# Kernel tuning notes

Hardware: AMD Instinct MI355X
Metric: run time of the kernel (lower is better)

## Reference

```python
import jax, jax.numpy as jnp
import numpy as np

N_QUBITS = 12
N_LAYERS = 6
BATCH = 2048
N_OUTPUTS = 2
C64 = jnp.complex64


def setup_inputs() -> dict:
    key = jax.random.key(0)
    k1, k2 = jax.random.split(key)
    x = jax.random.normal(k1, (BATCH, N_QUBITS), dtype=jnp.float32)
    # nn.Parameter: torch.randn(n_layers, n_qubits, 3) * 0.1
    weights = jax.random.normal(k2, (N_LAYERS, N_QUBITS, 3), dtype=jnp.float32) * 0.1
    return {"x": x, "weights": weights}


def _rx(t):
    # t: (...,) angles -> (..., 2, 2) RX matrices
    c = jnp.cos(t * 0.5).astype(C64)
    s = (-1j * jnp.sin(t * 0.5)).astype(C64)
    return jnp.stack([jnp.stack([c, s], -1), jnp.stack([s, c], -1)], -2)


def _ry(t):
    c = jnp.cos(t * 0.5).astype(C64)
    s = jnp.sin(t * 0.5).astype(C64)
    return jnp.stack([jnp.stack([c, -s], -1), jnp.stack([s, c], -1)], -2)


def _rz(t):
    e = jnp.exp(-0.5j * t).astype(C64)
    z = jnp.zeros_like(e)
    return jnp.stack([jnp.stack([e, z], -1), jnp.stack([z, jnp.conj(e)], -1)], -2)


def _rot(w):
    # PennyLane Rot(phi, theta, omega) = RZ(omega) @ RY(theta) @ RZ(phi); w: (n_qubits, 3)
    return _rz(w[:, 2]) @ _ry(w[:, 1]) @ _rz(w[:, 0])


def _apply_1q(state, gate, q):
    # state: (B, 2**n) complex; gate: (2,2) or (B,2,2); qubit q (wire 0 = MSB)
    B = state.shape[0]
    s = state.reshape(B, 2 ** q, 2, -1)
    if gate.ndim == 3:
        s = jnp.einsum('bij,bljr->blir', gate, s)
    else:
        s = jnp.einsum('ij,bljr->blir', gate, s)
    return s.reshape(B, -1)


def _apply_cnot(state, c, t, n):
    # control c, target t; flip target axis where control bit == 1
    B = state.shape[0]
    s = state.reshape((B,) + (2,) * n)
    ac, at = 1 + c, 1 + t
    s0 = jnp.take(s, 0, axis=ac)
    s1 = jnp.take(s, 1, axis=ac)
    at2 = at - 1 if at > ac else at
    s1 = jnp.flip(s1, axis=at2)
    s = jnp.stack([s0, s1], axis=ac)
    return s.reshape(B, -1)


def _layer(state, w, n):
    # strongly-entangling layer: Rot on every wire, then full CNOT entanglement
    rot = _rot(w)  # (n, 2, 2)
    for q in range(n):
        state = _apply_1q(state, rot[q], q)
    for i in range(n):
        for j in range(i + 1, n):
            state = _apply_cnot(state, i, j, n)
    return state


def _forward(x, weights):
    n = N_QUBITS
    B = x.shape[0]
    state = jnp.zeros((B, 2 ** n), C64).at[:, 0].set(1.0)
    # angle encoding: RX(x_q) on wire q (PennyLane AngleEmbedding default axis X)
    for q in range(n):
        state = _apply_1q(state, _rx(x[:, q]), q)
    layer_ckpt = jax.checkpoint(lambda s, w: _layer(s, w, n))
    for l in range(N_LAYERS):
        state = layer_ckpt(state, weights[l])
    # expval(PauliZ) on wires 0..n_outputs-1
    probs = state.real ** 2 + state.imag ** 2  # (B, 2**n)
    outs = []
    for k in range(N_OUTPUTS):
        p = probs.reshape(B, 2 ** k, 2, -1)
        outs.append(p[:, :, 0, :].sum((1, 2)) - p[:, :, 1, :].sum((1, 2)))
    return jnp.stack(outs, -1)  # (B, n_outputs)


def reference(x, weights):
    return _forward(x, weights)
```

## Files before the change

### kernel.cpp

```cpp
#include <hip/hip_runtime.h>
#include <math.h>

#define NQ 12
#define DIM 4096
#define NL 6
#define TPB 64


#define WS_WA0 0
#define WS_Z0  128
#define WS_W   256
#define WS_Z   896
#define WS_RYT 2176

typedef float f2 __attribute__((ext_vector_type(2)));

__device__ __forceinline__ f2 pk_mul(f2 a, f2 b) {
  f2 d; asm("v_pk_mul_f32 %0, %1, %2" : "=v"(d) : "v"(a), "v"(b)); return d;
}
__device__ __forceinline__ f2 pk_fma(f2 a, f2 b, f2 c) {
  f2 d; asm("v_pk_fma_f32 %0, %1, %2, %3" : "=v"(d) : "v"(a), "v"(b), "v"(c)); return d;
}
__device__ __forceinline__ f2 cmulp(f2 a, f2 c) {
  f2 r1, d;
  asm("v_pk_mul_f32 %0, %1, %2 op_sel:[0,0] op_sel_hi:[0,1]"
      : "=v"(r1) : "v"(a), "v"(c));
  asm("v_pk_fma_f32 %0, %1, %2, %3 op_sel:[1,1,0] op_sel_hi:[1,0,1] neg_lo:[1,0,0]"
      : "=v"(d) : "v"(a), "v"(c), "v"(r1));
  return d;
}

template<int BIT>
__device__ __forceinline__ void apply_ry64(f2 v[64], f2 cc, f2 ss) {
  #pragma unroll
  for (int j = 0; j < 64; ++j) {
    if (j & (1 << BIT)) continue;
    const int k = j | (1 << BIT);
    f2 a = v[j], b = v[k];
    f2 t1 = pk_mul(a, cc);
    f2 t2 = pk_mul(a, ss);
    f2 na; asm("v_pk_fma_f32 %0, %1, %2, %3 neg_lo:[1,0,0] neg_hi:[1,0,0]"
               : "=v"(na) : "v"(b), "v"(ss), "v"(t1));
    f2 nb = pk_fma(b, cc, t2);
    v[j] = na; v[k] = nb;
  }
}

__global__ __launch_bounds__(256)
void qprep_kernel(const float* __restrict__ w, float* __restrict__ ws) {
  const int t = threadIdx.x;
  const float HPI = 1.57079632679489662f;

  if (t < 64) {
    const int u = t;
    float f = 0.f;
    #pragma unroll
    for (int k = 0; k < 6; ++k) {
      float p = w[(0*NQ + (11-k))*3 + 0];
      f += ((u >> k) & 1) ? 0.5f*p : -0.5f*p;
    }
    f -= HPI * (float)__popc(u);
    float sv, cv; sincosf(f, &sv, &cv);
    ws[WS_WA0 + 2*u] = cv; ws[WS_WA0 + 2*u + 1] = sv;
  } else if (t < 128) {
    const int p_ = t - 64;
    float f = 0.f;
    #pragma unroll
    for (int k = 0; k < 6; ++k) {
      float p = w[(0*NQ + (5-k))*3 + 0];
      f += ((p_ >> k) & 1) ? 0.5f*p : -0.5f*p;
    }
    f -= HPI * (float)__popc(p_);
    float sv, cv; sincosf(f, &sv, &cv);
    ws[WS_Z0 + 2*p_] = cv; ws[WS_Z0 + 2*p_ + 1] = sv;
  }

  for (int idx = t; idx < 5*64; idx += 256) {
    const int l = idx >> 6, u = idx & 63;
    float f = 0.f;
    #pragma unroll
    for (int k = 0; k < 6; ++k) {
      float om = w[(l*NQ + (5-k))*3 + 2];
      f += ((u >> k) & 1) ? 0.5f*om : -0.5f*om;
    }
    const int gu = u ^ (u >> 1);
    #pragma unroll
    for (int k = 0; k < 6; ++k) {
      float ph = w[((l+1)*NQ + (5-k))*3 + 0];
      f += ((gu >> k) & 1) ? 0.5f*ph : -0.5f*ph;
    }
    float sv, cv; sincosf(f, &sv, &cv);
    ws[WS_W + 2*idx] = cv; ws[WS_W + 2*idx + 1] = sv;
  }

  for (int idx = t; idx < 5*2*64; idx += 256) {
    const int l = idx >> 7, h = (idx >> 6) & 1, p_ = idx & 63;
    float f = 0.f;
    #pragma unroll
    for (int k = 0; k < 6; ++k) {
      float om = w[(l*NQ + (11-k))*3 + 2];
      f += ((p_ >> k) & 1) ? 0.5f*om : -0.5f*om;
    }
    const int gp = (p_ ^ (p_ >> 1)) ^ (h << 5);
    #pragma unroll
    for (int k = 0; k < 6; ++k) {
      float ph = w[((l+1)*NQ + (11-k))*3 + 0];
      f += ((gp >> k) & 1) ? 0.5f*ph : -0.5f*ph;
    }
    float sv, cv; sincosf(f, &sv, &cv);
    ws[WS_Z + 2*idx] = cv; ws[WS_Z + 2*idx + 1] = sv;
  }

  if (t < NL*NQ) {
    float sv, cv; sincosf(0.5f*w[t*3 + 1], &sv, &cv);
    ((float4*)(ws + WS_RYT))[t] = make_float4(cv, cv, sv, sv);
  }
}

__global__ __launch_bounds__(TPB, 1)
void qsim12_kernel(const float* __restrict__ x, const float* __restrict__ ws,
                   float* __restrict__ out) {
  __shared__ __align__(16) float st[2*DIM];
  const int L = threadIdx.x;
  const int b = blockIdx.x;
  char* stb = (char*)st;

  float csx[NQ], csy[NQ];
  {
    float xv = (L < NQ) ? x[b*NQ + L] : 0.f;
    float sv, cv; sincosf(0.5f*xv, &sv, &cv);
    #pragma unroll
    for (int q = 0; q < NQ; ++q) {
      csx[q] = __int_as_float(__builtin_amdgcn_readlane(__float_as_int(cv), q));
      csy[q] = __int_as_float(__builtin_amdgcn_readlane(__float_as_int(sv), q));
    }
  }

  f2 v[64];

  {
    float rl = 1.f;
    #pragma unroll
    for (int k = 0; k < 6; ++k)
      rl *= ((L >> k) & 1) ? csy[11-k] : csx[11-k];
    float mlo[8], mhi[8];
    #pragma unroll
    for (int pm = 0; pm < 8; ++pm) {
      float a = ((pm >> 0) & 1) ? csy[5] : csx[5];
      a *= ((pm >> 1) & 1) ? csy[4] : csx[4];
      a *= ((pm >> 2) & 1) ? csy[3] : csx[3];
      mlo[pm] = a;
      float bb = ((pm >> 0) & 1) ? csy[2] : csx[2];
      bb *= ((pm >> 1) & 1) ? csy[1] : csx[1];
      bb *= ((pm >> 2) & 1) ? csy[0] : csx[0];
      mhi[pm] = bb;
    }
    const float2 wv = *(const float2*)(ws + WS_WA0 + 2*L);
    const f2 a0 = (f2){wv.x*rl, wv.y*rl};
    #pragma unroll
    for (int p = 0; p < 64; ++p) {
      const float2 zv = *(const float2*)(ws + WS_Z0 + 2*p);
      f2 ph = cmulp(a0, (f2){zv.x, zv.y});
      const float m = mlo[p & 7] * mhi[p >> 3];
      v[p] = pk_mul(ph, (f2){m, m});
    }
  }

  #define RY6(BIT, WQ) { const float4 r = *(const float4*)(ws + WS_RYT + 4*(l*NQ + (WQ))); \
      apply_ry64<BIT>(v, (f2){r.x, r.y}, (f2){r.z, r.w}); }

  #pragma unroll 1
  for (int l = 0; l < NL; ++l) {
    if (l > 0) {
      #pragma unroll
      for (int r = 0; r < 64; ++r)
        v[r] = *(const f2*)(stb + r*512 + ((L ^ (r & 62)) << 3));
    }
    RY6(0,5) RY6(1,4) RY6(2,3) RY6(3,2) RY6(4,1) RY6(5,0)

    #pragma unroll
    for (int m = 0; m < 32; ++m) {
      const int idx = (2*m) ^ (L & 62);
      *(float4*)(stb + L*512 + (idx << 3)) =
          make_float4(v[2*m].x, v[2*m].y, v[2*m+1].x, v[2*m+1].y);
    }
    __syncthreads();
    #pragma unroll
    for (int p = 0; p < 64; ++p)
      v[p] = *(const f2*)(stb + p*512 + ((L ^ (p & 62)) << 3));

    RY6(0,11) RY6(1,10) RY6(2,9) RY6(3,8) RY6(4,7) RY6(5,6)

    if (l < NL-1) {
      const float2 wv = *(const float2*)(ws + WS_W + (l*64 + L)*2);
      const f2 W = (f2){wv.x, wv.y};
      const float* zb = ws + WS_Z + ((l*2 + (L & 1))*64)*2;
      #pragma unroll
      for (int p0 = 0; p0 < 64; p0 += 8) {
        f2 z[8];
        #pragma unroll
        for (int q = 0; q < 8; ++q) {
          const float2 zv = *(const float2*)(zb + 2*(p0+q));
          z[q] = (f2){zv.x, zv.y};
        }
        #pragma unroll
        for (int q = 0; q < 8; ++q)
          v[p0+q] = cmulp(cmulp(v[p0+q], z[q]), W);
      }
      __syncthreads();

      const int Gh  = (L ^ (L >> 1)) & 63;
      const int hb5 = (L & 1) << 5;
      const int gsw = Gh & 62;
      #pragma unroll
      for (int m = 0; m < 32; ++m) {
        const int glo0 = ((2*m) ^ m) ^ hb5;
        const int e = glo0 & ~1;
        float4 q4;
        if (m & 1) q4 = make_float4(v[2*m+1].x, v[2*m+1].y, v[2*m].x, v[2*m].y);
        else       q4 = make_float4(v[2*m].x, v[2*m].y, v[2*m+1].x, v[2*m+1].y);
        *(float4*)(stb + Gh*512 + ((e ^ gsw) << 3)) = q4;
      }
      __syncthreads();
    }
  }

  float ssum = 0.f;
  #pragma unroll
  for (int p = 0; p < 64; ++p)
    ssum += v[p].x*v[p].x + v[p].y*v[p].y;
  float s0 = ((L >> 5) & 1) ? -ssum : ssum;
  float s1 = (((L >> 4) ^ (L >> 5)) & 1) ? -ssum : ssum;
  #pragma unroll
  for (int off = 32; off >= 1; off >>= 1) {
    s0 += __shfl_down(s0, off);
    s1 += __shfl_down(s1, off);
  }
  if (L == 0) { out[b*2 + 0] = s0; out[b*2 + 1] = s1; }
}

extern "C" void kernel_launch(void* const* d_in, const int* in_sizes, int n_in,
                              void* d_out, int out_size, void* d_ws, size_t ws_size,
                              hipStream_t stream) {
  const float* x = (const float*)d_in[0];
  const float* w = (const float*)d_in[1];
  float* out = (float*)d_out;
  float* ws = (float*)d_ws;
  int B = in_sizes[0] / NQ;
  qprep_kernel<<<1, 256, 0, stream>>>(w, ws);
  qsim12_kernel<<<B, TPB, 0, stream>>>(x, ws, out);
}
```

Baseline: 155.3 us.

## Replace shared-memory transposes with ds_bpermute cross-lane permutations

Both transposes between the low and high qubit halves now use per-register ds_bpermute lane shuffles, and so does the Gray-code CNOT permutation. That removes the shared-memory state buffer and the __syncthreads barriers. The Z phase table is copied into a small LDS array, and launch bounds are raised to 2 blocks per CU to improve occupancy. The RY update is reformulated with a lane-dependent sign so that each step maps onto the bpermute layout. Each bpermute of a complex value costs two LDS-path instructions, so there are many more of them per layer, and register pressure at the higher occupancy may cause spills.

Result: slower. 207.2 us (+33.4%).

```diff
diff --git a/kernel.cpp b/kernel.cpp
--- a/kernel.cpp
+++ b/kernel.cpp
@@ -2,7 +2,6 @@
 #include <math.h>
 
 #define NQ 12
-#define DIM 4096
 #define NL 6
 #define TPB 64
 
@@ -15,13 +14,13 @@
 
 typedef float f2 __attribute__((ext_vector_type(2)));
 
-__device__ __forceinline__ f2 pk_mul(f2 a, f2 b) {
+static __device__ __forceinline__ f2 pk_mul(f2 a, f2 b) {
   f2 d; asm("v_pk_mul_f32 %0, %1, %2" : "=v"(d) : "v"(a), "v"(b)); return d;
 }
-__device__ __forceinline__ f2 pk_fma(f2 a, f2 b, f2 c) {
+static __device__ __forceinline__ f2 pk_fma(f2 a, f2 b, f2 c) {
   f2 d; asm("v_pk_fma_f32 %0, %1, %2, %3" : "=v"(d) : "v"(a), "v"(b), "v"(c)); return d;
 }
-__device__ __forceinline__ f2 cmulp(f2 a, f2 c) {
+static __device__ __forceinline__ f2 cmulp(f2 a, f2 c) {
   f2 r1, d;
   asm("v_pk_mul_f32 %0, %1, %2 op_sel:[0,0] op_sel_hi:[0,1]"
       : "=v"(r1) : "v"(a), "v"(c));
@@ -29,20 +28,27 @@
       : "=v"(d) : "v"(a), "v"(c), "v"(r1));
   return d;
 }
+static __device__ __forceinline__ f2 bp2(int addr, f2 s) {
+  f2 d;
+  d.x = __int_as_float(__builtin_amdgcn_ds_bpermute(addr, __float_as_int(s.x)));
+  d.y = __int_as_float(__builtin_amdgcn_ds_bpermute(addr, __float_as_int(s.y)));
+  return d;
+}
 
 template<int BIT>
-__device__ __forceinline__ void apply_ry64(f2 v[64], f2 cc, f2 ss) {
+static __device__ __forceinline__ void apply_ry64(f2 v[64], f2 cc, f2 SS) {
   #pragma unroll
   for (int j = 0; j < 64; ++j) {
     if (j & (1 << BIT)) continue;
     const int k = j | (1 << BIT);
     f2 a = v[j], b = v[k];
     f2 t1 = pk_mul(a, cc);
-    f2 t2 = pk_mul(a, ss);
-    f2 na; asm("v_pk_fma_f32 %0, %1, %2, %3 neg_lo:[1,0,0] neg_hi:[1,0,0]"
-               : "=v"(na) : "v"(b), "v"(ss), "v"(t1));
-    f2 nb = pk_fma(b, cc, t2);
-    v[j] = na; v[k] = nb;
+    f2 t2 = pk_mul(b, cc);
+    v[j] = pk_fma(b, SS, t1);
+    f2 nb;
+    asm("v_pk_fma_f32 %0, %1, %2, %3 neg_lo:[1,0,0] neg_hi:[1,0,0]"
+        : "=v"(nb) : "v"(a), "v"(SS), "v"(t2));
+    v[k] = nb;
   }
 }
 
@@ -117,13 +123,24 @@
   }
 }
 
-__global__ __launch_bounds__(TPB, 1)
+#define STEP(DST, SRC) v[DST] = bp2(vgi ^ ((SRC) << 2), v[SRC]);
+#define CYC2(A,B) { f2 t_ = v[A]; STEP(A,B); v[B] = bp2(vgi ^ ((A) << 2), t_); }
+#define CYC4(A,B,C,D) { f2 t_ = v[A]; STEP(A,B); STEP(B,C); STEP(C,D); \
+                        v[D] = bp2(vgi ^ ((A) << 2), t_); }
+#define CYC8(A,B,C,D,E,F,G,H) { f2 t_ = v[A]; STEP(A,B); STEP(B,C); STEP(C,D); \
+                        STEP(D,E); STEP(E,F); STEP(F,G); STEP(G,H); \
+                        v[H] = bp2(vgi ^ ((A) << 2), t_); }
+
+__global__ __launch_bounds__(TPB, 2)
 void qsim12_kernel(const float* __restrict__ x, const float* __restrict__ ws,
                    float* __restrict__ out) {
-  __shared__ __align__(16) float st[2*DIM];
+  __shared__ __align__(16) float zt[5*2*64*2];
   const int L = threadIdx.x;
   const int b = blockIdx.x;
-  char* stb = (char*)st;
+
+  #pragma unroll
+  for (int i = 0; i < 10; ++i)
+    ((f2*)zt)[i*64 + L] = *(const f2*)(ws + WS_Z + 2*(i*64 + L));
 
   float csx[NQ], csy[NQ];
   {
@@ -137,91 +154,72 @@
   }
 
   f2 v[64];
+  const int lb = L << 2;
 
   {
     float rl = 1.f;
     #pragma unroll
     for (int k = 0; k < 6; ++k)
       rl *= ((L >> k) & 1) ? csy[11-k] : csx[11-k];
-    float mlo[8], mhi[8];
-    #pragma unroll
-    for (int pm = 0; pm < 8; ++pm) {
-      float a = ((pm >> 0) & 1) ? csy[5] : csx[5];
-      a *= ((pm >> 1) & 1) ? csy[4] : csx[4];
-      a *= ((pm >> 2) & 1) ? csy[3] : csx[3];
-      mlo[pm] = a;
-      float bb = ((pm >> 0) & 1) ? csy[2] : csx[2];
-      bb *= ((pm >> 1) & 1) ? csy[1] : csx[1];
-      bb *= ((pm >> 2) & 1) ? csy[0] : csx[0];
-      mhi[pm] = bb;
-    }
-    const float2 wv = *(const float2*)(ws + WS_WA0 + 2*L);
-    const f2 a0 = (f2){wv.x*rl, wv.y*rl};
-    #pragma unroll
-    for (int p = 0; p < 64; ++p) {
-      const float2 zv = *(const float2*)(ws + WS_Z0 + 2*p);
-      f2 ph = cmulp(a0, (f2){zv.x, zv.y});
-      const float m = mlo[p & 7] * mhi[p >> 3];
-      v[p] = pk_mul(ph, (f2){m, m});
-    }
-  }
-
-  #define RY6(BIT, WQ) { const float4 r = *(const float4*)(ws + WS_RYT + 4*(l*NQ + (WQ))); \
-      apply_ry64<BIT>(v, (f2){r.x, r.y}, (f2){r.z, r.w}); }
+    float mh = 1.f;
+    #pragma unroll
+    for (int k = 0; k < 6; ++k)
+      mh *= ((L >> k) & 1) ? csy[5-k] : csx[5-k];
+    const float2 z0 = *(const float2*)(ws + WS_Z0 + 2*L);
+    const float2 w0 = *(const float2*)(ws + WS_WA0 + 2*L);
+    const f2 zm = (f2){z0.x*mh, z0.y*mh};
+    const f2 a0 = (f2){w0.x*rl, w0.y*rl};
+    #pragma unroll
+    for (int d = 0; d < 64; ++d)
+      v[d] = cmulp(a0, bp2(lb ^ (d << 2), zm));
+  }
+
+  int gi = L; gi ^= gi >> 1; gi ^= gi >> 2; gi ^= gi >> 4;
+  const int vgi = gi << 2;
+  const bool oddl = (L & 1) != 0;
+
+  #define RYS(BIT, WQ) { \
+    const float4 r_ = *(const float4*)(ws + WS_RYT + 4*(l*NQ + (WQ)));   \
+    const float S_ = ((L >> (BIT)) & 1) ? r_.z : -r_.z;                  \
+    apply_ry64<BIT>(v, (f2){r_.x, r_.x}, (f2){S_, S_}); }
 
   #pragma unroll 1
   for (int l = 0; l < NL; ++l) {
-    if (l > 0) {
-      #pragma unroll
-      for (int r = 0; r < 64; ++r)
-        v[r] = *(const f2*)(stb + r*512 + ((L ^ (r & 62)) << 3));
-    }
-    RY6(0,5) RY6(1,4) RY6(2,3) RY6(3,2) RY6(4,1) RY6(5,0)
-
-    #pragma unroll
-    for (int m = 0; m < 32; ++m) {
-      const int idx = (2*m) ^ (L & 62);
-      *(float4*)(stb + L*512 + (idx << 3)) =
-          make_float4(v[2*m].x, v[2*m].y, v[2*m+1].x, v[2*m+1].y);
-    }
-    __syncthreads();
-    #pragma unroll
-    for (int p = 0; p < 64; ++p)
-      v[p] = *(const f2*)(stb + p*512 + ((L ^ (p & 62)) << 3));
-
-    RY6(0,11) RY6(1,10) RY6(2,9) RY6(3,8) RY6(4,7) RY6(5,6)
+    RYS(0,5) RYS(1,4) RYS(2,3) RYS(3,2) RYS(4,1) RYS(5,0)
+
+    #pragma unroll
+    for (int d = 0; d < 64; ++d)
+      v[d] = bp2(lb ^ (d << 2), v[d]);
+
+    RYS(0,11) RYS(1,10) RYS(2,9) RYS(3,8) RYS(4,7) RYS(5,6)
 
     if (l < NL-1) {
       const float2 wv = *(const float2*)(ws + WS_W + (l*64 + L)*2);
       const f2 W = (f2){wv.x, wv.y};
-      const float* zb = ws + WS_Z + ((l*2 + (L & 1))*64)*2;
+      const int zb = ((l*2 + (L & 1)) << 9) + (L << 3);
       #pragma unroll
-      for (int p0 = 0; p0 < 64; p0 += 8) {
-        f2 z[8];
-        #pragma unroll
-        for (int q = 0; q < 8; ++q) {
-          const float2 zv = *(const float2*)(zb + 2*(p0+q));
-          z[q] = (f2){zv.x, zv.y};
-        }
-        #pragma unroll
-        for (int q = 0; q < 8; ++q)
-          v[p0+q] = cmulp(cmulp(v[p0+q], z[q]), W);
+      for (int d = 0; d < 64; ++d) {
+        const f2 z = *(const f2*)((const char*)zt + (zb ^ (d << 3)));
+        v[d] = cmulp(cmulp(v[d], z), W);
       }
-      __syncthreads();
-
-      const int Gh  = (L ^ (L >> 1)) & 63;
-      const int hb5 = (L & 1) << 5;
-      const int gsw = Gh & 62;
+
       #pragma unroll
-      for (int m = 0; m < 32; ++m) {
-        const int glo0 = ((2*m) ^ m) ^ hb5;
-        const int e = glo0 & ~1;
-        float4 q4;
-        if (m & 1) q4 = make_float4(v[2*m+1].x, v[2*m+1].y, v[2*m].x, v[2*m].y);
-        else       q4 = make_float4(v[2*m].x, v[2*m].y, v[2*m+1].x, v[2*m+1].y);
-        *(float4*)(stb + Gh*512 + ((e ^ gsw) << 3)) = q4;
+      for (int r = 0; r < 32; ++r) {
+        const f2 a = v[r], c = v[63 - r];
+        v[r]      = oddl ? c : a;
+        v[63 - r] = oddl ? a : c;
       }
-      __syncthreads();
+      STEP(0,0) STEP(1,1)
+      CYC2(2,3)
+      CYC4(4,7,5,6)
+      CYC4(8,15,10,12)
+      CYC4(9,14,11,13)
+      CYC8(16,31,21,25,17,30,20,24)
+      CYC8(18,28,23,26,19,29,22,27)
+      CYC8(32,63,42,51,34,60,40,48)
+      CYC8(33,62,43,50,35,61,41,49)
+      CYC8(36,56,47,53,38,59,45,54)
+      CYC8(37,57,46,52,39,58,44,55)
     }
   }
 
```

## Pack two batch elements per block sharing one LDS buffer in turns

Applied to the files above, without the earlier changes.

Each 128-thread block now simulates two batch elements, one per wavefront. The two waves share a single 32KB shared-memory transpose buffer and take turns, separated by block barriers. The aim is to double the number of resident waves per CU without growing LDS, since LDS was the limit before, so that one wave's compute can overlap with the other's LDS exchange. In exchange, each wave now waits for the other wave's exchange, which serialises those phases, and the launch bounds ask for two blocks per CU, which may press on register allocation for the 64-entry complex register array.

After: 162.5 us. 1.05x slower.

```diff
diff --git a/kernel.cpp b/kernel.cpp
--- a/kernel.cpp
+++ b/kernel.cpp
@@ -4,7 +4,7 @@
 #define NQ 12
 #define DIM 4096
 #define NL 6
-#define TPB 64
+#define TPB 128
 
 
 #define WS_WA0 0
@@ -15,13 +15,13 @@
 
 typedef float f2 __attribute__((ext_vector_type(2)));
 
-__device__ __forceinline__ f2 pk_mul(f2 a, f2 b) {
+static __device__ __forceinline__ f2 pk_mul(f2 a, f2 b) {
   f2 d; asm("v_pk_mul_f32 %0, %1, %2" : "=v"(d) : "v"(a), "v"(b)); return d;
 }
-__device__ __forceinline__ f2 pk_fma(f2 a, f2 b, f2 c) {
+static __device__ __forceinline__ f2 pk_fma(f2 a, f2 b, f2 c) {
   f2 d; asm("v_pk_fma_f32 %0, %1, %2, %3" : "=v"(d) : "v"(a), "v"(b), "v"(c)); return d;
 }
-__device__ __forceinline__ f2 cmulp(f2 a, f2 c) {
+static __device__ __forceinline__ f2 cmulp(f2 a, f2 c) {
   f2 r1, d;
   asm("v_pk_mul_f32 %0, %1, %2 op_sel:[0,0] op_sel_hi:[0,1]"
       : "=v"(r1) : "v"(a), "v"(c));
@@ -31,7 +31,7 @@
 }
 
 template<int BIT>
-__device__ __forceinline__ void apply_ry64(f2 v[64], f2 cc, f2 ss) {
+static __device__ __forceinline__ void apply_ry64(f2 v[64], f2 cc, f2 ss) {
   #pragma unroll
   for (int j = 0; j < 64; ++j) {
     if (j & (1 << BIT)) continue;
@@ -117,17 +117,50 @@
   }
 }
 
-__global__ __launch_bounds__(TPB, 1)
+#define T1_SESSION() do {                                                    \
+    _Pragma("unroll")                                                        \
+    for (int m = 0; m < 32; ++m) {                                           \
+      const int idx = (2*m) ^ (L & 62);                                      \
+      *(float4*)(stb + L*512 + (idx << 3)) =                                 \
+          make_float4(v[2*m].x, v[2*m].y, v[2*m+1].x, v[2*m+1].y);           \
+    }                                                                        \
+    asm volatile("s_waitcnt lgkmcnt(0)" ::: "memory");                       \
+    _Pragma("unroll")                                                        \
+    for (int p = 0; p < 64; ++p)                                             \
+      v[p] = *(const f2*)(stb + p*512 + ((L ^ (p & 62)) << 3));              \
+  } while (0)
+
+#define FOLD_SESSION() do {                                                  \
+    const int Gh  = (L ^ (L >> 1)) & 63;                                     \
+    const int hb5 = (L & 1) << 5;                                            \
+    const int gsw = Gh & 62;                                                 \
+    _Pragma("unroll")                                                        \
+    for (int m = 0; m < 32; ++m) {                                           \
+      const int glo0 = ((2*m) ^ m) ^ hb5;                                    \
+      const int e_ = glo0 & ~1;                                              \
+      float4 q4;                                                             \
+      if (m & 1) q4 = make_float4(v[2*m+1].x, v[2*m+1].y, v[2*m].x, v[2*m].y);\
+      else       q4 = make_float4(v[2*m].x, v[2*m].y, v[2*m+1].x, v[2*m+1].y);\
+      *(float4*)(stb + Gh*512 + ((e_ ^ gsw) << 3)) = q4;                     \
+    }                                                                        \
+    asm volatile("s_waitcnt lgkmcnt(0)" ::: "memory");                       \
+    _Pragma("unroll")                                                        \
+    for (int r = 0; r < 64; ++r)                                             \
+      v[r] = *(const f2*)(stb + r*512 + ((L ^ (r & 62)) << 3));              \
+  } while (0)
+
+__global__ __launch_bounds__(TPB, 2)
 void qsim12_kernel(const float* __restrict__ x, const float* __restrict__ ws,
                    float* __restrict__ out) {
   __shared__ __align__(16) float st[2*DIM];
-  const int L = threadIdx.x;
-  const int b = blockIdx.x;
+  const int L = threadIdx.x & 63;
+  const int w = threadIdx.x >> 6;
+  const int e = blockIdx.x*2 + w;
   char* stb = (char*)st;
 
   float csx[NQ], csy[NQ];
   {
-    float xv = (L < NQ) ? x[b*NQ + L] : 0.f;
+    float xv = (L < NQ) ? x[e*NQ + L] : 0.f;
     float sv, cv; sincosf(0.5f*xv, &sv, &cv);
     #pragma unroll
     for (int q = 0; q < NQ; ++q) {
@@ -171,23 +204,12 @@
 
   #pragma unroll 1
   for (int l = 0; l < NL; ++l) {
-    if (l > 0) {
-      #pragma unroll
-      for (int r = 0; r < 64; ++r)
-        v[r] = *(const f2*)(stb + r*512 + ((L ^ (r & 62)) << 3));
-    }
     RY6(0,5) RY6(1,4) RY6(2,3) RY6(3,2) RY6(4,1) RY6(5,0)
 
-    #pragma unroll
-    for (int m = 0; m < 32; ++m) {
-      const int idx = (2*m) ^ (L & 62);
-      *(float4*)(stb + L*512 + (idx << 3)) =
-          make_float4(v[2*m].x, v[2*m].y, v[2*m+1].x, v[2*m+1].y);
-    }
     __syncthreads();
-    #pragma unroll
-    for (int p = 0; p < 64; ++p)
-      v[p] = *(const f2*)(stb + p*512 + ((L ^ (p & 62)) << 3));
+    if (w == 0) T1_SESSION();
+    __syncthreads();
+    if (w == 1) T1_SESSION();
 
     RY6(0,11) RY6(1,10) RY6(2,9) RY6(3,8) RY6(4,7) RY6(5,6)
 
@@ -207,21 +229,11 @@
         for (int q = 0; q < 8; ++q)
           v[p0+q] = cmulp(cmulp(v[p0+q], z[q]), W);
       }
+
       __syncthreads();
-
-      const int Gh  = (L ^ (L >> 1)) & 63;
-      const int hb5 = (L & 1) << 5;
-      const int gsw = Gh & 62;
-      #pragma unroll
-      for (int m = 0; m < 32; ++m) {
-        const int glo0 = ((2*m) ^ m) ^ hb5;
-        const int e = glo0 & ~1;
-        float4 q4;
-        if (m & 1) q4 = make_float4(v[2*m+1].x, v[2*m+1].y, v[2*m].x, v[2*m].y);
-        else       q4 = make_float4(v[2*m].x, v[2*m].y, v[2*m+1].x, v[2*m+1].y);
-        *(float4*)(stb + Gh*512 + ((e ^ gsw) << 3)) = q4;
-      }
+      if (w == 0) FOLD_SESSION();
       __syncthreads();
+      if (w == 1) FOLD_SESSION();
     }
   }
 
@@ -236,7 +248,7 @@
     s0 += __shfl_down(s0, off);
     s1 += __shfl_down(s1, off);
   }
-  if (L == 0) { out[b*2 + 0] = s0; out[b*2 + 1] = s1; }
+  if (L == 0) { out[e*2 + 0] = s0; out[e*2 + 1] = s1; }
 }
 
 extern "C" void kernel_launch(void* const* d_in, const int* in_sizes, int n_in,
@@ -248,5 +260,5 @@
   float* ws = (float*)d_ws;
   int B = in_sizes[0] / NQ;
   qprep_kernel<<<1, 256, 0, stream>>>(w, ws);
-  qsim12_kernel<<<B, TPB, 0, stream>>>(x, ws, out);
-}
+  qsim12_kernel<<<B/2, TPB, 0, stream>>>(x, ws, out);
+}
```
